# Kernel optimization log

Measured on AMD Instinct MI355X. Metric: run time of the kernel, lower is better.

Reference implementation:

```python
import jax, jax.numpy as jnp
import numpy as np

N = 50000
E = 800000
DES, TW, NUMP, CATP = 768, 768, 4, 3
EMB = 384
THIRD = EMB // 3  # 128


def _lin(key, fan_in, fan_out):
    k1, k2 = jax.random.split(key)
    bound = 1.0 / np.sqrt(fan_in)
    W = jax.random.uniform(k1, (fan_in, fan_out), jnp.float32, -bound, bound)
    b = jax.random.uniform(k2, (fan_out,), jnp.float32, -bound, bound)
    return W, b


def setup_inputs() -> dict:
    key = jax.random.key(0)
    ks = jax.random.split(key, 16)
    des = jax.random.normal(ks[0], (N, DES), jnp.float32)
    tweet = jax.random.normal(ks[1], (N, TW), jnp.float32)
    num_prop = jax.random.normal(ks[2], (N, NUMP), jnp.float32)
    cat_prop = jax.random.normal(ks[3], (N, CATP), jnp.float32)
    edge_index = jax.random.randint(ks[4], (2, E), 0, N, jnp.int64)
    W_des, b_des = _lin(ks[5], DES, THIRD)
    W_num, b_num = _lin(ks[6], NUMP, THIRD)
    W_cat, b_cat = _lin(ks[7], CATP, THIRD)
    W_in, b_in = _lin(ks[8], EMB, EMB)
    W_g1, b_g1 = _lin(ks[9], EMB, EMB)
    W_g2, b_g2 = _lin(ks[10], EMB, EMB)
    W_o1, b_o1 = _lin(ks[11], EMB, EMB)
    W_o2, b_o2 = _lin(ks[12], EMB, 2)
    return dict(des=des, tweet=tweet, num_prop=num_prop, cat_prop=cat_prop,
                edge_index=edge_index,
                W_des=W_des, b_des=b_des, W_num=W_num, b_num=b_num,
                W_cat=W_cat, b_cat=b_cat, W_in=W_in, b_in=b_in,
                W_g1=W_g1, b_g1=b_g1, W_g2=W_g2, b_g2=b_g2,
                W_o1=W_o1, b_o1=b_o1, W_o2=W_o2, b_o2=b_o2)


def _leaky(x):
    return jax.nn.leaky_relu(x, 0.01)


def _gcn_conv(x, edge_index, W, b):
    # PyG GCNConv: x' = D^{-1/2} (A + I) D^{-1/2} (x W) + b
    src, dst = edge_index[0], edge_index[1]
    x = x @ W  # [N, out]
    n = x.shape[0]
    deg = jax.ops.segment_sum(jnp.ones(src.shape[0], x.dtype), dst, num_segments=n) + 1.0  # self-loop
    dinv = jax.lax.rsqrt(deg)  # deg >= 1
    norm = dinv[src] * dinv[dst]  # [E]
    msg = x[src] * norm[:, None]  # [E, out] gather
    agg = jax.ops.segment_sum(msg, dst, num_segments=n)  # scatter-add
    agg = agg + x * (dinv * dinv)[:, None]  # self-loop contribution
    return agg + b


def reference(des, tweet, num_prop, cat_prop, edge_index,
              W_des, b_des, W_num, b_num, W_cat, b_cat, W_in, b_in,
              W_g1, b_g1, W_g2, b_g2, W_o1, b_o1, W_o2, b_o2):
    # eval mode: dropout is identity
    d = _leaky(des @ W_des + b_des)
    n = _leaky(num_prop @ W_num + b_num)
    c = _leaky(cat_prop @ W_cat + b_cat)
    x = jnp.concatenate((d, n, c), axis=1)  # [N, EMB]
    x = _leaky(x @ W_in + b_in)
    x = _gcn_conv(x, edge_index, W_g1, b_g1)
    x = _gcn_conv(x, edge_index, W_g2, b_g2)
    x = _leaky(x @ W_o1 + b_o1)
    return x @ W_o2 + b_o2  # [N, 2]
```

## Files before the change

### kernel.cpp

```cpp
#include <hip/hip_runtime.h>
#include <hip/hip_bf16.h>
#include <cstdint>

#define NFEAT 384
#define DESK 768
#define THIRD 128

typedef __bf16 bf16x8 __attribute__((ext_vector_type(8)));
typedef unsigned short u16x8 __attribute__((ext_vector_type(8)));
typedef unsigned short u16x4 __attribute__((ext_vector_type(4)));
typedef float f32x16 __attribute__((ext_vector_type(16)));
typedef _Float16 h16x2 __attribute__((ext_vector_type(2)));

__device__ __forceinline__ float leaky(float x) { return x > 0.f ? x : 0.01f * x; }

__device__ __forceinline__ unsigned short bfhi(float x) {
  unsigned int u = __float_as_uint(x);
  u += 0x7fffu + ((u >> 16) & 1u);
  return (unsigned short)(u >> 16);
}
__device__ __forceinline__ float bf2f(unsigned short h) {
  return __uint_as_float(((unsigned int)h) << 16);
}
__device__ __forceinline__ void bsplit(float x, unsigned short& h,
                                       unsigned short& l) {
  h = bfhi(x);
  l = bfhi(x - bf2f(h));
}

#define MFMA(a, b, c) __builtin_amdgcn_mfma_f32_32x32x16_bf16(a, b, c, 0, 0, 0)

template <int AFP32, int EPI, int BM>
__global__ __launch_bounds__(256, 2) void mfma_gemm(
    const float* __restrict__ Af, const unsigned short* __restrict__ Ahi,
    const unsigned short* __restrict__ Alo,
    const unsigned short* __restrict__ BThi,
    const unsigned short* __restrict__ BTlo, _Float16* __restrict__ Ch16,
    unsigned short* __restrict__ Chi, unsigned short* __restrict__ Clo,
    const float* __restrict__ bias, int M, int K, int ldc) {
  __shared__ unsigned short AhiL[2][4 * BM * 8];
  __shared__ unsigned short AloL[2][4 * BM * 8];
  __shared__ unsigned short BhiL[2][4 * 128 * 8];
  __shared__ unsigned short BloL[2][4 * 128 * 8];
  const int tid = threadIdx.x;
  const int lane = tid & 63;
  const int w = tid >> 6;
  constexpr int MR = BM / 64;
  const int wm = (w >> 1) * (BM / 2);
  const int wn = (w & 1) * 64;
  const int lm = lane & 31, lk = lane >> 5;

  int bx = blockIdx.x, by = blockIdx.y;
  if (gridDim.y == 3) {
    int lin = by * gridDim.x + bx;
    int ng = gridDim.x >> 3;
    int full = ng * 24;
    if (lin < full) {
      int g = lin / 24, x = lin - g * 24;
      bx = g * 8 + (x & 7);
      by = x >> 3;
    } else {
      int rem = lin - full;
      int mrem = gridDim.x - (ng << 3);
      bx = (ng << 3) + rem % mrem;
      by = rem / mrem;
    }
  }
  const int m_base = bx * BM, n_base = by * 128;

  f32x16 acc[MR][2];
#pragma unroll
  for (int mi = 0; mi < MR; mi++)
#pragma unroll
    for (int nt = 0; nt < 2; nt++)
#pragma unroll
      for (int r = 0; r < 16; r++) acc[mi][nt][r] = 0.f;

  constexpr int AIT_F = BM / 32;
  constexpr int AIT_H = BM / 64;
  float4 pa[3][AIT_F];
  u16x8 pah[3][AIT_H], pal[3][AIT_H];
  u16x8 pbh[3][2], pbl[3][2];

  auto loadA = [&](int kt, int s) {
    if (AFP32) {
#pragma unroll
      for (int it = 0; it < AIT_F; it++) {
        int r = (tid >> 3) + it * 32;
        int gr = m_base + r;
        float4 av = make_float4(0.f, 0.f, 0.f, 0.f);
        if (gr < M) av = *(const float4*)&Af[(size_t)gr * K + kt + (tid & 7) * 4];
        pa[s][it] = av;
      }
    } else {
#pragma unroll
      for (int it = 0; it < AIT_H; it++) {
        int r = (tid >> 2) + it * 64;
        int gr = m_base + r;
        u16x8 vh = {0, 0, 0, 0, 0, 0, 0, 0};
        u16x8 vl = {0, 0, 0, 0, 0, 0, 0, 0};
        if (gr < M) {
          vh = *(const u16x8*)&Ahi[(size_t)gr * K + kt + (tid & 3) * 8];
          vl = *(const u16x8*)&Alo[(size_t)gr * K + kt + (tid & 3) * 8];
        }
        pah[s][it] = vh;
        pal[s][it] = vl;
      }
    }
  };
  auto loadB = [&](int kt, int s) {
#pragma unroll
    for (int it = 0; it < 2; it++) {
      int n = (tid >> 2) + it * 64;
      pbh[s][it] = *(const u16x8*)&BThi[(size_t)(n_base + n) * K + kt + (tid & 3) * 8];
      pbl[s][it] = *(const u16x8*)&BTlo[(size_t)(n_base + n) * K + kt + (tid & 3) * 8];
    }
  };
  auto storeLDS = [&](int s, int b) {
    if (AFP32) {
#pragma unroll
      for (int it = 0; it < AIT_F; it++) {
        int r = (tid >> 3) + it * 32;
        int q = tid & 7;
        float4 av = pa[s][it];
        unsigned short h0, h1, h2, h3, l0, l1, l2, l3;
        bsplit(av.x, h0, l0);
        bsplit(av.y, h1, l1);
        bsplit(av.z, h2, l2);
        bsplit(av.w, h3, l3);
        int base = ((q >> 1) * BM + r) * 8 + (q & 1) * 4;
        u16x4 th;
        th.x = h0; th.y = h1; th.z = h2; th.w = h3;
        u16x4 tl;
        tl.x = l0; tl.y = l1; tl.z = l2; tl.w = l3;
        *(u16x4*)&AhiL[b][base] = th;
        *(u16x4*)&AloL[b][base] = tl;
      }
    } else {
#pragma unroll
      for (int it = 0; it < AIT_H; it++) {
        int r = (tid >> 2) + it * 64;
        int kb = tid & 3;
        *(u16x8*)&AhiL[b][(kb * BM + r) * 8] = pah[s][it];
        *(u16x8*)&AloL[b][(kb * BM + r) * 8] = pal[s][it];
      }
    }
#pragma unroll
    for (int it = 0; it < 2; it++) {
      int n = (tid >> 2) + it * 64;
      int kb = tid & 3;
      *(u16x8*)&BhiL[b][(kb * 128 + n) * 8] = pbh[s][it];
      *(u16x8*)&BloL[b][(kb * 128 + n) * 8] = pbl[s][it];
    }
  };
  auto compute = [&](int b) {
#pragma unroll
    for (int ks = 0; ks < 2; ks++) {
      int kb = 2 * ks + lk;
      bf16x8 ah[MR], al[MR];
#pragma unroll
      for (int mi = 0; mi < MR; mi++) {
        ah[mi] = __builtin_bit_cast(
            bf16x8, *(const u16x8*)&AhiL[b][(kb * BM + wm + mi * 32 + lm) * 8]);
        al[mi] = __builtin_bit_cast(
            bf16x8, *(const u16x8*)&AloL[b][(kb * BM + wm + mi * 32 + lm) * 8]);
      }
      bf16x8 bh0 = __builtin_bit_cast(
          bf16x8, *(const u16x8*)&BhiL[b][(kb * 128 + wn + lm) * 8]);
      bf16x8 bh1 = __builtin_bit_cast(
          bf16x8, *(const u16x8*)&BhiL[b][(kb * 128 + wn + 32 + lm) * 8]);
      bf16x8 bl0 = __builtin_bit_cast(
          bf16x8, *(const u16x8*)&BloL[b][(kb * 128 + wn + lm) * 8]);
      bf16x8 bl1 = __builtin_bit_cast(
          bf16x8, *(const u16x8*)&BloL[b][(kb * 128 + wn + 32 + lm) * 8]);
#pragma unroll
      for (int mi = 0; mi < MR; mi++) {
        acc[mi][0] = MFMA(ah[mi], bh0, acc[mi][0]);
        acc[mi][1] = MFMA(ah[mi], bh1, acc[mi][1]);
        acc[mi][0] = MFMA(ah[mi], bl0, acc[mi][0]);
        acc[mi][1] = MFMA(ah[mi], bl1, acc[mi][1]);
        acc[mi][0] = MFMA(al[mi], bh0, acc[mi][0]);
        acc[mi][1] = MFMA(al[mi], bh1, acc[mi][1]);
      }
    }
  };

  loadA(0, 0);
  loadB(0, 0);
  loadA(32, 1);
  loadB(32, 1);
  loadA(64, 2);
  loadB(64, 2);
  storeLDS(0, 0);
  __syncthreads();

  const int NK = K >> 5;
  for (int m6 = 0; m6 < NK / 6; m6++) {
#pragma unroll
    for (int ph = 0; ph < 6; ph++) {
      const int i = m6 * 6 + ph;
      if (i + 1 < NK) storeLDS((ph + 1) % 3, (ph + 1) & 1);
      if (i + 3 < NK) {
        loadA((i + 3) << 5, ph % 3);
        loadB((i + 3) << 5, ph % 3);
      }
      compute(ph & 1);
      __syncthreads();
    }
  }

  const int colb = n_base + wn;
#pragma unroll
  for (int mi = 0; mi < MR; mi++) {
#pragma unroll
    for (int nt = 0; nt < 2; nt++) {
      f32x16 v = acc[mi][nt];
      int col = colb + nt * 32 + lm;
      float bv = (EPI == 0) ? bias[col] : 0.f;
      int rb = m_base + wm + mi * 32 + 4 * lk;
#pragma unroll
      for (int rg = 0; rg < 16; rg++) {
        int row = rb + (rg & 3) + 8 * (rg >> 2);
        if (row < M) {
          float x = v[rg];
          if (EPI == 0) {
            x = leaky(x + bv);
            unsigned short h, l;
            bsplit(x, h, l);
            Chi[(size_t)row * ldc + col] = h;
            Clo[(size_t)row * ldc + col] = l;
          } else {
            Ch16[(size_t)row * ldc + col] = (_Float16)x;
          }
        }
      }
    }
  }
}

__global__ __launch_bounds__(256) void split_transpose_b(
    const float* __restrict__ s0, unsigned short* __restrict__ h0,
    unsigned short* __restrict__ l0, const float* __restrict__ s1,
    unsigned short* __restrict__ h1, unsigned short* __restrict__ l1,
    const float* __restrict__ s2, unsigned short* __restrict__ h2,
    unsigned short* __restrict__ l2) {
  int z = blockIdx.z;
  const float* src = z == 0 ? s0 : (z == 1 ? s1 : s2);
  unsigned short* dsthi = z == 0 ? h0 : (z == 1 ? h1 : h2);
  unsigned short* dstlo = z == 0 ? l0 : (z == 1 ? l1 : l2);
  int R = z == 0 ? 768 : 384;
  int C = z == 0 ? 128 : 384;
  int c0 = blockIdx.x * 32, r0 = blockIdx.y * 32;
  if (c0 >= C || r0 >= R) return;
  __shared__ float tile[32][33];
  int tx = threadIdx.x & 31, ty = threadIdx.x >> 5;
#pragma unroll
  for (int i = 0; i < 4; i++)
    tile[ty + i * 8][tx] = src[(size_t)(r0 + ty + i * 8) * C + c0 + tx];
  __syncthreads();
#pragma unroll
  for (int i = 0; i < 4; i++) {
    int c = c0 + ty + i * 8, r = r0 + tx;
    float v = tile[tx][ty + i * 8];
    unsigned short h, l;
    bsplit(v, h, l);
    dsthi[(size_t)c * R + r] = h;
    dstlo[(size_t)c * R + r] = l;
  }
}

__global__ __launch_bounds__(256) void gemm384(const float* __restrict__ A,
                                               const float* __restrict__ B,
                                               float* __restrict__ C) {
  __shared__ float As[16][68];
  __shared__ float Bs[16][64];
  const int tid = threadIdx.x;
  const int mb = blockIdx.x * 64;
  const int nb = blockIdx.y * 64;
  float acc[4][4] = {};
  const int arow = tid >> 2, akq = tid & 3;
  const int brow = tid >> 4, bc4 = tid & 15;
  const int m0 = (tid >> 4) * 4, n0 = (tid & 15) * 4;
  for (int kk = 0; kk < 384; kk += 16) {
    float4 av = *(const float4*)&A[(mb + arow) * 384 + kk + akq * 4];
    As[akq * 4 + 0][arow] = av.x;
    As[akq * 4 + 1][arow] = av.y;
    As[akq * 4 + 2][arow] = av.z;
    As[akq * 4 + 3][arow] = av.w;
    *(float4*)&Bs[brow][bc4 * 4] =
        *(const float4*)&B[(kk + brow) * 384 + nb + bc4 * 4];
    __syncthreads();
#pragma unroll
    for (int k = 0; k < 16; k++) {
      float4 a4 = *(const float4*)&As[k][m0];
      float4 b4 = *(const float4*)&Bs[k][n0];
      float a[4] = {a4.x, a4.y, a4.z, a4.w};
      float b[4] = {b4.x, b4.y, b4.z, b4.w};
#pragma unroll
      for (int i = 0; i < 4; i++)
#pragma unroll
        for (int j = 0; j < 4; j++) acc[i][j] = fmaf(a[i], b[j], acc[i][j]);
    }
    __syncthreads();
  }
#pragma unroll
  for (int i = 0; i < 4; i++)
#pragma unroll
    for (int j = 0; j < 4; j++)
      C[(mb + m0 + i) * 384 + nb + n0 + j] = acc[i][j];
}

__global__ void uv_kernel(const float* __restrict__ T1,
                          const float* __restrict__ W_o1,
                          const float* __restrict__ b_g1,
                          const float* __restrict__ b_g2,
                          const float* __restrict__ b_o1, float* __restrict__ u,
                          float* __restrict__ v) {
  int j = blockIdx.x * blockDim.x + threadIdx.x;
  if (j < 384) {
    float su = 0.f, sv = 0.f;
    for (int k = 0; k < 384; k++) {
      su = fmaf(T1[k * 384 + j], b_g1[k], su);
      sv = fmaf(W_o1[k * 384 + j], b_g2[k], sv);
    }
    u[j] = su;
    v[j] = sv + b_o1[j];
  }
}

__global__ __launch_bounds__(256) void numcat_kernel(
    const float* __restrict__ num, const float* __restrict__ cat,
    const float* __restrict__ Wn, const float* __restrict__ bn,
    const float* __restrict__ Wc, const float* __restrict__ bc,
    unsigned short* __restrict__ x0hi, unsigned short* __restrict__ x0lo,
    int N) {
  int c = threadIdx.x;
  for (int i = blockIdx.x; i < N; i += gridDim.x) {
    float val;
    if (c < 128) {
      val = bn[c];
      val = fmaf(num[i * 4 + 0], Wn[0 * 128 + c], val);
      val = fmaf(num[i * 4 + 1], Wn[1 * 128 + c], val);
      val = fmaf(num[i * 4 + 2], Wn[2 * 128 + c], val);
      val = fmaf(num[i * 4 + 3], Wn[3 * 128 + c], val);
    } else {
      int cc = c - 128;
      val = bc[cc];
      val = fmaf(cat[i * 3 + 0], Wc[0 * 128 + cc], val);
      val = fmaf(cat[i * 3 + 1], Wc[1 * 128 + cc], val);
      val = fmaf(cat[i * 3 + 2], Wc[2 * 128 + cc], val);
    }
    val = leaky(val);
    unsigned short h, l;
    bsplit(val, h, l);
    size_t o = (size_t)i * NFEAT + 128 + c;
    x0hi[o] = h;
    x0lo[o] = l;
  }
}

__global__ void count_kernel(const int* __restrict__ dst, int* __restrict__ deg,
                             int E) {
  int e = blockIdx.x * blockDim.x + threadIdx.x;
  if (e < E) atomicAdd(&deg[dst[e]], 1);
}

__global__ void scan_reduce(const int* __restrict__ deg,
                            int* __restrict__ partial, int N) {
  __shared__ int sm[512];
  int i = blockIdx.x * 512 + threadIdx.x;
  sm[threadIdx.x] = (i < N) ? deg[i] : 0;
  __syncthreads();
  for (int off = 256; off; off >>= 1) {
    if (threadIdx.x < off) sm[threadIdx.x] += sm[threadIdx.x + off];
    __syncthreads();
  }
  if (threadIdx.x == 0) partial[blockIdx.x] = sm[0];
}

__global__ void scan_top(int* partial, int nb) {
  if (threadIdx.x == 0 && blockIdx.x == 0) {
    int run = 0;
    for (int b = 0; b < nb; b++) {
      int t = partial[b];
      partial[b] = run;
      run += t;
    }
  }
}

__global__ void scan_down(const int* __restrict__ deg,
                          const int* __restrict__ partial,
                          int* __restrict__ offsets, int* __restrict__ cursor,
                          float* __restrict__ dinv, int N, int E) {
  __shared__ int sm[512];
  int t = threadIdx.x;
  int i = blockIdx.x * 512 + t;
  int val = (i < N) ? deg[i] : 0;
  sm[t] = val;
  __syncthreads();
  for (int off = 1; off < 512; off <<= 1) {
    int add = (t >= off) ? sm[t - off] : 0;
    __syncthreads();
    sm[t] += add;
    __syncthreads();
  }
  if (i < N) {
    int ex = partial[blockIdx.x] + sm[t] - val;
    offsets[i] = ex;
    cursor[i] = ex;
    dinv[i] = 1.0f / sqrtf((float)val + 1.0f);
  }
  if (i == 0) offsets[N] = E;
}

__global__ void fill_kernel(const int* __restrict__ src,
                            const int* __restrict__ dst,
                            int* __restrict__ cursor,
                            int* __restrict__ csr_off,
                            float* __restrict__ csr_w,
                            const float* __restrict__ dinv, int E) {
  int e = blockIdx.x * blockDim.x + threadIdx.x;
  if (e < E) {
    int s = src[e], d = dst[e];
    int slot = atomicAdd(&cursor[d], 1);
    csr_off[slot] = s * NFEAT;
    csr_w[slot] = dinv[s] * dinv[d];
  }
}

template <int WRITE_S, int FINAL>
__global__ __launch_bounds__(192) void agg_kernel(
    const _Float16* __restrict__ xin, _Float16* __restrict__ xout,
    const int* __restrict__ offsets, const int* __restrict__ csr_off,
    const float* __restrict__ csr_w, const float* __restrict__ dinv,
    float* __restrict__ sout, const float* __restrict__ svec,
    const float* __restrict__ uvec, const float* __restrict__ vvec,
    const float* __restrict__ W_o2, const float* __restrict__ b_o2,
    float* __restrict__ out, int N) {
  const int t = threadIdx.x;
  const int ff = 2 * t;
  __shared__ int ssrc[192];
  __shared__ float sw[192];
  __shared__ float red[3][2];
  float u0 = 0.f, u1 = 0.f, vc0 = 0.f, vc1 = 0.f;
  float w00 = 0.f, w01 = 0.f, w10 = 0.f, w11 = 0.f, bo0 = 0.f, bo1 = 0.f;
  if (FINAL) {
    u0 = uvec[ff];
    u1 = uvec[ff + 1];
    vc0 = vvec[ff];
    vc1 = vvec[ff + 1];
    w00 = W_o2[ff * 2 + 0];
    w01 = W_o2[ff * 2 + 1];
    w10 = W_o2[(ff + 1) * 2 + 0];
    w11 = W_o2[(ff + 1) * 2 + 1];
    bo0 = b_o2[0];
    bo1 = b_o2[1];
  }
  for (int i = blockIdx.x; i < N; i += gridDim.x) {
    int beg = offsets[i], end = offsets[i + 1];
    float di = dinv[i];
    float dii = di * di;
    h16x2 xs = *(const h16x2*)&xin[(size_t)i * NFEAT + ff];
    float A0x = dii * (float)xs.x, A0y = dii * (float)xs.y;
    float A1x = 0.f, A1y = 0.f, A2x = 0.f, A2y = 0.f, A3x = 0.f, A3y = 0.f;
    float wsum = dii;
    for (int j0 = beg; j0 < end; j0 += 192) {
      int cnt = min(192, end - j0);
      if (t < cnt) {
        ssrc[t] = csr_off[j0 + t];
        sw[t] = csr_w[j0 + t];
      }
      __syncthreads();
      int j = 0;
      for (; j + 8 <= cnt; j += 8) {
        int o0 = ssrc[j + 0], o1 = ssrc[j + 1], o2 = ssrc[j + 2],
            o3 = ssrc[j + 3];
        int o4 = ssrc[j + 4], o5 = ssrc[j + 5], o6 = ssrc[j + 6],
            o7 = ssrc[j + 7];
        float w0 = sw[j + 0], w1 = sw[j + 1], w2 = sw[j + 2], w3 = sw[j + 3];
        float w4 = sw[j + 4], w5 = sw[j + 5], w6 = sw[j + 6], w7 = sw[j + 7];
        h16x2 v0 = *(const h16x2*)&xin[o0 + ff];
        h16x2 v1 = *(const h16x2*)&xin[o1 + ff];
        h16x2 v2 = *(const h16x2*)&xin[o2 + ff];
        h16x2 v3 = *(const h16x2*)&xin[o3 + ff];
        h16x2 v4 = *(const h16x2*)&xin[o4 + ff];
        h16x2 v5 = *(const h16x2*)&xin[o5 + ff];
        h16x2 v6 = *(const h16x2*)&xin[o6 + ff];
        h16x2 v7 = *(const h16x2*)&xin[o7 + ff];
        A0x = fmaf(w0, (float)v0.x, A0x);
        A0y = fmaf(w0, (float)v0.y, A0y);
        A1x = fmaf(w1, (float)v1.x, A1x);
        A1y = fmaf(w1, (float)v1.y, A1y);
        A2x = fmaf(w2, (float)v2.x, A2x);
        A2y = fmaf(w2, (float)v2.y, A2y);
        A3x = fmaf(w3, (float)v3.x, A3x);
        A3y = fmaf(w3, (float)v3.y, A3y);
        A0x = fmaf(w4, (float)v4.x, A0x);
        A0y = fmaf(w4, (float)v4.y, A0y);
        A1x = fmaf(w5, (float)v5.x, A1x);
        A1y = fmaf(w5, (float)v5.y, A1y);
        A2x = fmaf(w6, (float)v6.x, A2x);
        A2y = fmaf(w6, (float)v6.y, A2y);
        A3x = fmaf(w7, (float)v7.x, A3x);
        A3y = fmaf(w7, (float)v7.y, A3y);
        if (WRITE_S) wsum += ((w0 + w1) + (w2 + w3)) + ((w4 + w5) + (w6 + w7));
      }
      for (; j < cnt; j++) {
        float wj = sw[j];
        h16x2 vj = *(const h16x2*)&xin[ssrc[j] + ff];
        A0x = fmaf(wj, (float)vj.x, A0x);
        A0y = fmaf(wj, (float)vj.y, A0y);
        if (WRITE_S) wsum += wj;
      }
      __syncthreads();
    }
    float ax = (A0x + A1x) + (A2x + A3x);
    float ay = (A0y + A1y) + (A2y + A3y);
    if (!FINAL) {
      h16x2 r;
      r.x = (_Float16)ax;
      r.y = (_Float16)ay;
      *(h16x2*)&xout[(size_t)i * NFEAT + ff] = r;
      if (WRITE_S && t == 0) sout[i] = wsum;
    } else {
      float si = svec[i];
      float q0 = leaky(ax + si * u0 + vc0);
      float q1 = leaky(ay + si * u1 + vc1);
      float c0 = q0 * w00 + q1 * w10;
      float c1 = q0 * w01 + q1 * w11;
#pragma unroll
      for (int off2 = 32; off2; off2 >>= 1) {
        c0 += __shfl_down(c0, off2, 64);
        c1 += __shfl_down(c1, off2, 64);
      }
      int wid = t >> 6, lane2 = t & 63;
      if (lane2 == 0) {
        red[wid][0] = c0;
        red[wid][1] = c1;
      }
      __syncthreads();
      if (t == 0) {
        out[i * 2 + 0] = red[0][0] + red[1][0] + red[2][0] + bo0;
        out[i * 2 + 1] = red[0][1] + red[1][1] + red[2][1] + bo1;
      }
    }
  }
}

extern "C" void kernel_launch(void* const* d_in, const int* in_sizes, int n_in,
                              void* d_out, int out_size, void* d_ws,
                              size_t ws_size, hipStream_t stream) {
  const float* des = (const float*)d_in[0];
  const float* num_prop = (const float*)d_in[2];
  const float* cat_prop = (const float*)d_in[3];
  const int* edge = (const int*)d_in[4];
  const float* W_des = (const float*)d_in[5];
  const float* b_des = (const float*)d_in[6];
  const float* W_num = (const float*)d_in[7];
  const float* b_num = (const float*)d_in[8];
  const float* W_cat = (const float*)d_in[9];
  const float* b_cat = (const float*)d_in[10];
  const float* W_in = (const float*)d_in[11];
  const float* b_in = (const float*)d_in[12];
  const float* W_g1 = (const float*)d_in[13];
  const float* b_g1 = (const float*)d_in[14];
  const float* W_g2 = (const float*)d_in[15];
  const float* b_g2 = (const float*)d_in[16];
  const float* W_o1 = (const float*)d_in[17];
  const float* b_o1 = (const float*)d_in[18];
  const float* W_o2 = (const float*)d_in[19];
  const float* b_o2 = (const float*)d_in[20];
  float* out = (float*)d_out;

  const int N = in_sizes[0] / DESK;
  const int E = in_sizes[4] / 2;
  const int* esrc = edge;
  const int* edst = edge + E;

  char* ws = (char*)d_ws;
  size_t off = 0;
  auto alloc = [&](size_t n) {
    off = (off + 255) & ~(size_t)255;
    size_t o = off;
    off += n;
    return o;
  };
  float* bufA = (float*)(ws + alloc((size_t)N * NFEAT * 4));
  float* bufB = (float*)(ws + alloc((size_t)N * NFEAT * 4));
  int* deg = (int*)(ws + alloc((size_t)N * 4));
  int* offsets = (int*)(ws + alloc((size_t)(N + 1) * 4));
  int* cursor = (int*)(ws + alloc((size_t)N * 4));
  int* partial = (int*)(ws + alloc(1024 * 4));
  float* dinv = (float*)(ws + alloc((size_t)N * 4));
  float* svec = (float*)(ws + alloc((size_t)N * 4));
  int* csr_off = (int*)(ws + alloc((size_t)E * 4));
  float* csr_w = (float*)(ws + alloc((size_t)E * 4));
  float* T1 = (float*)(ws + alloc(384 * 384 * 4));
  float* Mmat = (float*)(ws + alloc(384 * 384 * 4));
  float* uvec = (float*)(ws + alloc(384 * 4));
  float* vvec = (float*)(ws + alloc(384 * 4));
  unsigned short* WdThi = (unsigned short*)(ws + alloc(768 * 128 * 2));
  unsigned short* WdTlo = (unsigned short*)(ws + alloc(768 * 128 * 2));
  unsigned short* WiThi = (unsigned short*)(ws + alloc(384 * 384 * 2));
  unsigned short* WiTlo = (unsigned short*)(ws + alloc(384 * 384 * 2));
  unsigned short* MmThi = (unsigned short*)(ws + alloc(384 * 384 * 2));
  unsigned short* MmTlo = (unsigned short*)(ws + alloc(384 * 384 * 2));
  (void)ws_size;
  (void)n_in;
  (void)out_size;

  unsigned short* x0hi = (unsigned short*)bufA;
  unsigned short* x0lo = x0hi + (size_t)N * NFEAT;
  unsigned short* x1hi = (unsigned short*)bufB;
  unsigned short* x1lo = x1hi + (size_t)N * NFEAT;
  _Float16* yb = (_Float16*)bufA;
  _Float16* w1 = (_Float16*)bufB;

  hipMemsetAsync(deg, 0, (size_t)N * 4, stream);

  dim3 g6(6, 6);
  gemm384<<<g6, 256, 0, stream>>>(W_g2, W_o1, T1);
  gemm384<<<g6, 256, 0, stream>>>(W_g1, T1, Mmat);
  uv_kernel<<<2, 256, 0, stream>>>(T1, W_o1, b_g1, b_g2, b_o1, uvec, vvec);
  split_transpose_b<<<dim3(12, 24, 3), 256, 0, stream>>>(
      W_des, WdThi, WdTlo, W_in, WiThi, WiTlo, Mmat, MmThi, MmTlo);

  const int MT = (N + 127) / 128;
  const int MT64 = (N + 63) / 64;
  mfma_gemm<1, 0, 64><<<dim3(MT64, 1), 256, 0, stream>>>(
      des, nullptr, nullptr, WdThi, WdTlo, nullptr, x0hi, x0lo, b_des, N, DESK,
      NFEAT);
  numcat_kernel<<<1024, 256, 0, stream>>>(num_prop, cat_prop, W_num, b_num,
                                          W_cat, b_cat, x0hi, x0lo, N);
  mfma_gemm<0, 0, 128><<<dim3(MT, 3), 256, 0, stream>>>(
      nullptr, x0hi, x0lo, WiThi, WiTlo, nullptr, x1hi, x1lo, b_in, N, NFEAT,
      NFEAT);
  mfma_gemm<0, 1, 128><<<dim3(MT, 3), 256, 0, stream>>>(
      nullptr, x1hi, x1lo, MmThi, MmTlo, yb, nullptr, nullptr, nullptr, N,
      NFEAT, NFEAT);

  const int EB = (E + 255) / 256;
  count_kernel<<<EB, 256, 0, stream>>>(edst, deg, E);
  const int NB = (N + 511) / 512;
  scan_reduce<<<NB, 512, 0, stream>>>(deg, partial, N);
  scan_top<<<1, 64, 0, stream>>>(partial, NB);
  scan_down<<<NB, 512, 0, stream>>>(deg, partial, offsets, cursor, dinv, N, E);
  fill_kernel<<<EB, 256, 0, stream>>>(esrc, edst, cursor, csr_off, csr_w, dinv,
                                      E);

  agg_kernel<1, 0><<<4096, 192, 0, stream>>>(
      yb, w1, offsets, csr_off, csr_w, dinv, svec, nullptr, nullptr, nullptr,
      nullptr, nullptr, nullptr, N);
  agg_kernel<0, 1><<<4096, 192, 0, stream>>>(
      w1, nullptr, offsets, csr_off, csr_w, dinv, nullptr, svec, uvec, vvec,
      W_o2, b_o2, out, N);
}
```

Baseline: 935.3 us.

## Swizzle LDS tiles in MFMA GEMM and single-buffer the des GEMM

Adds an XOR swizzle on the LDS row index for both the A and B hi/lo tiles, so the strided 16-byte reads and writes hit fewer bank conflicts. Adds a DBUF template flag. With it off, the BM=64 des-projection GEMM uses a single LDS buffer and syncs before and after each compute step, which halves its LDS footprint so more blocks can fit per CU. The 128-row GEMMs keep double buffering. The trade-off is an extra barrier per k-step in the des GEMM, which reduces overlap between LDS stores and MFMA work.

```diff
diff --git a/kernel.cpp b/kernel.cpp
--- a/kernel.cpp
+++ b/kernel.cpp
@@ -28,9 +28,13 @@
   l = bfhi(x - bf2f(h));
 }
 
+__device__ __forceinline__ int swz(int kb, int row, int ROWS) {
+  return (kb * ROWS + (row ^ (kb << 1))) * 8;
+}
+
 #define MFMA(a, b, c) __builtin_amdgcn_mfma_f32_32x32x16_bf16(a, b, c, 0, 0, 0)
 
-template <int AFP32, int EPI, int BM>
+template <int AFP32, int EPI, int BM, int DBUF>
 __global__ __launch_bounds__(256, 2) void mfma_gemm(
     const float* __restrict__ Af, const unsigned short* __restrict__ Ahi,
     const unsigned short* __restrict__ Alo,
@@ -38,10 +42,10 @@
     const unsigned short* __restrict__ BTlo, _Float16* __restrict__ Ch16,
     unsigned short* __restrict__ Chi, unsigned short* __restrict__ Clo,
     const float* __restrict__ bias, int M, int K, int ldc) {
-  __shared__ unsigned short AhiL[2][4 * BM * 8];
-  __shared__ unsigned short AloL[2][4 * BM * 8];
-  __shared__ unsigned short BhiL[2][4 * 128 * 8];
-  __shared__ unsigned short BloL[2][4 * 128 * 8];
+  __shared__ unsigned short AhiL[DBUF + 1][4 * BM * 8];
+  __shared__ unsigned short AloL[DBUF + 1][4 * BM * 8];
+  __shared__ unsigned short BhiL[DBUF + 1][4 * 128 * 8];
+  __shared__ unsigned short BloL[DBUF + 1][4 * 128 * 8];
   const int tid = threadIdx.x;
   const int lane = tid & 63;
   const int w = tid >> 6;
@@ -128,7 +132,7 @@
         bsplit(av.y, h1, l1);
         bsplit(av.z, h2, l2);
         bsplit(av.w, h3, l3);
-        int base = ((q >> 1) * BM + r) * 8 + (q & 1) * 4;
+        int base = swz(q >> 1, r, BM) + (q & 1) * 4;
         u16x4 th;
         th.x = h0; th.y = h1; th.z = h2; th.w = h3;
         u16x4 tl;
@@ -141,16 +145,16 @@
       for (int it = 0; it < AIT_H; it++) {
         int r = (tid >> 2) + it * 64;
         int kb = tid & 3;
-        *(u16x8*)&AhiL[b][(kb * BM + r) * 8] = pah[s][it];
-        *(u16x8*)&AloL[b][(kb * BM + r) * 8] = pal[s][it];
+        *(u16x8*)&AhiL[b][swz(kb, r, BM)] = pah[s][it];
+        *(u16x8*)&AloL[b][swz(kb, r, BM)] = pal[s][it];
       }
     }
 #pragma unroll
     for (int it = 0; it < 2; it++) {
       int n = (tid >> 2) + it * 64;
       int kb = tid & 3;
-      *(u16x8*)&BhiL[b][(kb * 128 + n) * 8] = pbh[s][it];
-      *(u16x8*)&BloL[b][(kb * 128 + n) * 8] = pbl[s][it];
+      *(u16x8*)&BhiL[b][swz(kb, n, 128)] = pbh[s][it];
+      *(u16x8*)&BloL[b][swz(kb, n, 128)] = pbl[s][it];
     }
   };
   auto compute = [&](int b) {
@@ -161,18 +165,18 @@
 #pragma unroll
       for (int mi = 0; mi < MR; mi++) {
         ah[mi] = __builtin_bit_cast(
-            bf16x8, *(const u16x8*)&AhiL[b][(kb * BM + wm + mi * 32 + lm) * 8]);
+            bf16x8, *(const u16x8*)&AhiL[b][swz(kb, wm + mi * 32 + lm, BM)]);
         al[mi] = __builtin_bit_cast(
-            bf16x8, *(const u16x8*)&AloL[b][(kb * BM + wm + mi * 32 + lm) * 8]);
+            bf16x8, *(const u16x8*)&AloL[b][swz(kb, wm + mi * 32 + lm, BM)]);
       }
       bf16x8 bh0 = __builtin_bit_cast(
-          bf16x8, *(const u16x8*)&BhiL[b][(kb * 128 + wn + lm) * 8]);
+          bf16x8, *(const u16x8*)&BhiL[b][swz(kb, wn + lm, 128)]);
       bf16x8 bh1 = __builtin_bit_cast(
-          bf16x8, *(const u16x8*)&BhiL[b][(kb * 128 + wn + 32 + lm) * 8]);
+          bf16x8, *(const u16x8*)&BhiL[b][swz(kb, wn + 32 + lm, 128)]);
       bf16x8 bl0 = __builtin_bit_cast(
-          bf16x8, *(const u16x8*)&BloL[b][(kb * 128 + wn + lm) * 8]);
+          bf16x8, *(const u16x8*)&BloL[b][swz(kb, wn + lm, 128)]);
       bf16x8 bl1 = __builtin_bit_cast(
-          bf16x8, *(const u16x8*)&BloL[b][(kb * 128 + wn + 32 + lm) * 8]);
+          bf16x8, *(const u16x8*)&BloL[b][swz(kb, wn + 32 + lm, 128)]);
 #pragma unroll
       for (int mi = 0; mi < MR; mi++) {
         acc[mi][0] = MFMA(ah[mi], bh0, acc[mi][0]);
@@ -185,27 +189,44 @@
     }
   };
 
+  const int NK = K >> 5;
   loadA(0, 0);
   loadB(0, 0);
   loadA(32, 1);
   loadB(32, 1);
   loadA(64, 2);
   loadB(64, 2);
-  storeLDS(0, 0);
-  __syncthreads();
-
-  const int NK = K >> 5;
-  for (int m6 = 0; m6 < NK / 6; m6++) {
-#pragma unroll
-    for (int ph = 0; ph < 6; ph++) {
-      const int i = m6 * 6 + ph;
-      if (i + 1 < NK) storeLDS((ph + 1) % 3, (ph + 1) & 1);
-      if (i + 3 < NK) {
-        loadA((i + 3) << 5, ph % 3);
-        loadB((i + 3) << 5, ph % 3);
-      }
-      compute(ph & 1);
-      __syncthreads();
+
+  if (DBUF) {
+    storeLDS(0, 0);
+    __syncthreads();
+    for (int m6 = 0; m6 < NK / 6; m6++) {
+#pragma unroll
+      for (int ph = 0; ph < 6; ph++) {
+        const int i = m6 * 6 + ph;
+        if (i + 1 < NK) storeLDS((ph + 1) % 3, (ph + 1) & 1);
+        if (i + 3 < NK) {
+          loadA((i + 3) << 5, ph % 3);
+          loadB((i + 3) << 5, ph % 3);
+        }
+        compute(ph & 1);
+        __syncthreads();
+      }
+    }
+  } else {
+    for (int m3 = 0; m3 < NK / 3; m3++) {
+#pragma unroll
+      for (int ph = 0; ph < 3; ph++) {
+        const int i = m3 * 3 + ph;
+        storeLDS(ph, 0);
+        __syncthreads();
+        if (i + 3 < NK) {
+          loadA((i + 3) << 5, ph);
+          loadB((i + 3) << 5, ph);
+        }
+        compute(0);
+        __syncthreads();
+      }
     }
   }
 
@@ -628,15 +649,15 @@
 
   const int MT = (N + 127) / 128;
   const int MT64 = (N + 63) / 64;
-  mfma_gemm<1, 0, 64><<<dim3(MT64, 1), 256, 0, stream>>>(
+  mfma_gemm<1, 0, 64, 0><<<dim3(MT64, 1), 256, 0, stream>>>(
       des, nullptr, nullptr, WdThi, WdTlo, nullptr, x0hi, x0lo, b_des, N, DESK,
       NFEAT);
   numcat_kernel<<<1024, 256, 0, stream>>>(num_prop, cat_prop, W_num, b_num,
                                           W_cat, b_cat, x0hi, x0lo, N);
-  mfma_gemm<0, 0, 128><<<dim3(MT, 3), 256, 0, stream>>>(
+  mfma_gemm<0, 0, 128, 1><<<dim3(MT, 3), 256, 0, stream>>>(
       nullptr, x0hi, x0lo, WiThi, WiTlo, nullptr, x1hi, x1lo, b_in, N, NFEAT,
       NFEAT);
-  mfma_gemm<0, 1, 128><<<dim3(MT, 3), 256, 0, stream>>>(
+  mfma_gemm<0, 1, 128, 1><<<dim3(MT, 3), 256, 0, stream>>>(
       nullptr, x1hi, x1lo, MmThi, MmTlo, yb, nullptr, nullptr, nullptr, N,
       NFEAT, NFEAT);
 
```

After: 912.1 us, median of 2. 1.03x faster.
